# Kernel tuning notes

Hardware: AMD Instinct MI355X
Metric: run time of the kernel (lower is better)

## Reference

```python
import jax, jax.numpy as jnp
import numpy as np

B, T, HU, C = 256, 128, 512, 64

def setup_inputs() -> dict:
    key = jax.random.key(0)
    k = jax.random.split(key, 8)
    H = jax.random.normal(k[0], (B, T, HU), dtype=jnp.float32)
    y = jax.random.randint(k[1], (B, T), 0, C)
    y_len = jax.random.randint(k[2], (B,), 1, T + 1).astype(jnp.int32)
    y_mask = (jnp.arange(T)[None, :] < y_len[:, None]).astype(jnp.float32)
    xav = float(np.sqrt(6.0 / (3 * HU + C)))
    W = jax.random.uniform(k[3], (C, 3 * HU), minval=-xav, maxval=xav, dtype=jnp.float32)
    b = jnp.zeros((C,), dtype=jnp.float32)
    start_transitions = jax.random.uniform(k[4], (C,), minval=-1.0, maxval=1.0, dtype=jnp.float32)
    end_transitions = jax.random.uniform(k[5], (C,), minval=-1.0, maxval=1.0, dtype=jnp.float32)
    transitions = jax.random.uniform(k[6], (C, C), minval=-1.0, maxval=1.0, dtype=jnp.float32)
    return {"H": H, "W": W, "b": b, "start_transitions": start_transitions,
            "end_transitions": end_transitions, "transitions": transitions,
            "y": y, "y_mask": y_mask, "y_len": y_len}

def _crf_ll(H, W, b, start_transitions, end_transitions, transitions, y, y_mask, y_len):
    Bn, Tn, hu = H.shape
    zeros = jnp.zeros((Bn, 1, hu), H.dtype)
    prev = jnp.concatenate([zeros, H[:, :-1, :]], axis=1)
    nxt = jnp.concatenate([H[:, 1:, :], zeros], axis=1)
    context = jnp.concatenate([prev, H, nxt], axis=-1)            # [B,T,3h]
    scores = jnp.einsum('bth,ch->btc', context, W) + b            # [B,T,C]

    # numerator (gold path score)
    em_sel = jnp.take_along_axis(scores, y[..., None], axis=2)[..., 0]  # [B,T]
    num = start_transitions[y[:, 0]]
    num = num + jnp.sum(em_sel[:, :-1] * y_mask[:, :-1], axis=1)
    num = num + jnp.sum(transitions[y[:, :-1], y[:, 1:]] * y_mask[:, 1:], axis=1)
    last_tags = jnp.take_along_axis(y, (y_len - 1)[:, None].astype(y.dtype), axis=1)[:, 0]
    num = num + end_transitions[last_tags]
    num = num + jnp.take_along_axis(scores[:, -1, :], last_tags[:, None], axis=1)[:, 0] * y_mask[:, -1]

    # partition (log Z) via masked logsumexp scan
    em_t = jnp.transpose(scores, (1, 0, 2))   # [T,B,C]
    m_t = y_mask.T                            # [T,B]
    lp0 = start_transitions[None, :] + em_t[0]
    def step(lp, inp):
        em, m = inp
        new = jax.nn.logsumexp(lp[:, :, None] + transitions[None, :, :] + em[:, None, :], axis=1)
        lp = new * m[:, None] + lp * (1.0 - m[:, None])
        return lp, None
    lp, _ = jax.lax.scan(step, lp0, (em_t[1:], m_t[1:]))
    logZ = jax.nn.logsumexp(lp + end_transitions[None, :], axis=1)
    return num - logZ                          # [B]

def reference(H, W, b, start_transitions, end_transitions, transitions, y, y_mask, y_len):
    return _crf_ll(H, W, b, start_transitions, end_transitions, transitions, y, y_mask, y_len)
```

## Files before the change

kernel.cpp:

```cpp
#include <hip/hip_runtime.h>

typedef __attribute__((ext_vector_type(8))) short short8;
typedef __attribute__((ext_vector_type(4))) float f32x4;

__device__ __forceinline__ unsigned pk_rne(float a, float b) {
  unsigned short ha = __builtin_bit_cast(unsigned short, (_Float16)a);
  unsigned short hb = __builtin_bit_cast(unsigned short, (_Float16)b);
  return (unsigned)ha | ((unsigned)hb << 16);
}
__device__ __forceinline__ unsigned short f2bf(float x) {
  unsigned int u = __float_as_uint(x);
  u += 0x7FFFu + ((u >> 16) & 1u);
  return (unsigned short)(u >> 16);
}
__device__ __forceinline__ float bf2f(unsigned short h) {
  return __uint_as_float(((unsigned)h) << 16);
}
__device__ __forceinline__ unsigned pk_bf(float a, float b) {
  unsigned r;
  asm("v_cvt_pk_bf16_f32 %0, %1, %2" : "=v"(r) : "v"(a), "v"(b));
  return r;
}
__device__ __forceinline__ unsigned scale_bf_pair(unsigned w, float s) {
  float f0 = __uint_as_float(w << 16) * s;
  float f1 = __uint_as_float(w & 0xFFFF0000u) * s;
  return pk_bf(f0, f1);
}

__global__ __launch_bounds__(512) void crf_fused_kernel(
    const float* __restrict__ H, const float* __restrict__ W,
    const float* __restrict__ bias,
    const float* __restrict__ startT, const float* __restrict__ endT,
    const float* __restrict__ trans,
    const int* __restrict__ y, const int* __restrict__ y_len,
    float* __restrict__ out)
{
  __shared__ __align__(16) float smem[25088];
  __shared__ __align__(16) unsigned char EAbuf[8192];
  __shared__ __align__(16) float sc[128][68];
  __shared__ float scm[128];
  __shared__ float emy[128];
  __shared__ __align__(16) float ubuf[64];
  __shared__ float numsh;
  unsigned char* stg = (unsigned char*)smem;
  float* P = smem;
  unsigned char* Mbase = (unsigned char*)smem;

  const int b    = blockIdx.x;
  const int tid  = threadIdx.x;
  const int lane = tid & 63;
  const int wid  = tid >> 6;
  const int wm   = wid >> 2;
  const int wn   = wid & 3;

  f32x4 acc[4][3] = {};
  const float* Hb = H + (size_t)b * (128 * 512);
  const int len = y_len[b];
  const int* yb = y + b * 128;

  float4 areg[4], breg[6];
  int aRow[4], aK4[4], bN[6], bK4[6];
  #pragma unroll
  for (int it = 0; it < 4; ++it) { int i = it * 512 + tid; aRow[it] = i >> 4; aK4[it] = i & 15; }
  #pragma unroll
  for (int it = 0; it < 6; ++it) { int i = it * 512 + tid; bN[it] = i >> 4; bK4[it] = i & 15; }
  #pragma unroll
  for (int it = 0; it < 4; ++it)
    areg[it] = ((const float4*)(Hb + aRow[it] * 512))[aK4[it]];
  #pragma unroll
  for (int it = 0; it < 6; ++it)
    breg[it] = ((const float4*)(W + (bN[it] & 63) * 1536 + (bN[it] >> 6) * 512))[bK4[it]];

  #pragma unroll
  for (int it = 0; it < 2; ++it) {
    int idx = it * 512 + tid;
    int c = idx >> 4, c4 = idx & 15;
    float4 v = ((const float4*)trans)[idx];
    #pragma unroll
    for (int e = 0; e < 4; ++e) {
      int cp = c4 * 4 + e;
      float val = __expf(((const float*)&v)[e] - 1.0f);
      *(unsigned short*)(EAbuf + cp * 128 + ((2 * c) ^ ((cp & 7) << 4))) = f2bf(val);
    }
  }

  #pragma unroll
  for (int it = 0; it < 4; ++it) {
    float4 v = areg[it];
    uint2 o; o.x = pk_rne(v.x, v.y); o.y = pk_rne(v.z, v.w);
    *(uint2*)(stg + aRow[it] * 128 + ((aK4[it] * 8) ^ ((aRow[it] & 7) << 4))) = o;
  }
  #pragma unroll
  for (int it = 0; it < 6; ++it) {
    float4 v = breg[it];
    uint2 o; o.x = pk_rne(v.x, v.y); o.y = pk_rne(v.z, v.w);
    *(uint2*)(stg + 16384 + bN[it] * 128 + ((bK4[it] * 8) ^ ((bN[it] & 7) << 4))) = o;
  }
  __syncthreads();

  for (int kk = 0; kk < 8; ++kk) {
    unsigned char* aTc = stg + (kk & 1) * 40960;
    unsigned char* bTc = aTc + 16384;
    if (kk < 7) {
      #pragma unroll
      for (int it = 0; it < 4; ++it)
        areg[it] = ((const float4*)(Hb + aRow[it] * 512 + (kk + 1) * 64))[aK4[it]];
      #pragma unroll
      for (int it = 0; it < 6; ++it)
        breg[it] = ((const float4*)(W + (bN[it] & 63) * 1536 + (bN[it] >> 6) * 512 + (kk + 1) * 64))[bK4[it]];
    }
    #pragma unroll
    for (int ks = 0; ks < 2; ++ks) {
      const int kbyte = ks * 64 + ((lane >> 4) << 4);
      short8 ah[4], bh[3];
      #pragma unroll
      for (int m = 0; m < 4; ++m) {
        int row = wm * 64 + m * 16 + (lane & 15);
        ah[m] = *(const short8*)(aTc + row * 128 + (kbyte ^ ((row & 7) << 4)));
      }
      #pragma unroll
      for (int n = 0; n < 3; ++n) {
        int col = wn * 48 + n * 16 + (lane & 15);
        bh[n] = *(const short8*)(bTc + col * 128 + (kbyte ^ ((col & 7) << 4)));
      }
      #pragma unroll
      for (int m = 0; m < 4; ++m)
        #pragma unroll
        for (int n = 0; n < 3; ++n)
          asm("v_mfma_f32_16x16x32_f16 %0, %1, %2, %0"
              : "+v"(acc[m][n]) : "v"(ah[m]), "v"(bh[n]));
    }
    if (kk < 7) {
      unsigned char* aTn = stg + ((kk + 1) & 1) * 40960;
      unsigned char* bTn = aTn + 16384;
      #pragma unroll
      for (int it = 0; it < 4; ++it) {
        float4 v = areg[it];
        uint2 o; o.x = pk_rne(v.x, v.y); o.y = pk_rne(v.z, v.w);
        *(uint2*)(aTn + aRow[it] * 128 + ((aK4[it] * 8) ^ ((aRow[it] & 7) << 4))) = o;
      }
      #pragma unroll
      for (int it = 0; it < 6; ++it) {
        float4 v = breg[it];
        uint2 o; o.x = pk_rne(v.x, v.y); o.y = pk_rne(v.z, v.w);
        *(uint2*)(bTn + bN[it] * 128 + ((bK4[it] * 8) ^ ((bN[it] & 7) << 4))) = o;
      }
    }
    __syncthreads();
  }

  #pragma unroll
  for (int m = 0; m < 4; ++m)
    #pragma unroll
    for (int n = 0; n < 3; ++n) {
      int row0 = wm * 64 + m * 16 + ((lane >> 4) << 2);
      int col  = wn * 48 + n * 16 + (lane & 15);
      #pragma unroll
      for (int j = 0; j < 4; ++j)
        P[(row0 + j) * 196 + col] = acc[m][n][j];
    }
  __syncthreads();

  #pragma unroll
  for (int it = 0; it < 4; ++it) {
    int i4 = it * 512 + tid;
    int t = i4 >> 4, c4 = i4 & 15;
    float4 s = *(const float4*)(P + t * 196 + 64 + c4 * 4);
    float4 bb = ((const float4*)bias)[c4];
    s.x += bb.x; s.y += bb.y; s.z += bb.z; s.w += bb.w;
    if (t > 0) {
      float4 g = *(const float4*)(P + (t - 1) * 196 + c4 * 4);
      s.x += g.x; s.y += g.y; s.z += g.z; s.w += g.w;
    }
    if (t < 127) {
      float4 g = *(const float4*)(P + (t + 1) * 196 + 128 + c4 * 4);
      s.x += g.x; s.y += g.y; s.z += g.z; s.w += g.w;
    }
    float m4 = fmaxf(fmaxf(s.x, s.y), fmaxf(s.z, s.w));
    #pragma unroll
    for (int o = 1; o < 16; o <<= 1) m4 = fmaxf(m4, __shfl_xor(m4, o, 64));
    if ((lane & 15) == 0) scm[t] = m4;
    int yt = yb[t];
    if ((yt >> 2) == c4) {
      int r = yt & 3;
      emy[t] = (r == 0) ? s.x : (r == 1) ? s.y : (r == 2) ? s.z : s.w;
    }
    float4 e;
    e.x = __expf(s.x - m4); e.y = __expf(s.y - m4);
    e.z = __expf(s.z - m4); e.w = __expf(s.w - m4);
    *(float4*)(&sc[t][c4 * 4]) = e;
  }
  __syncthreads();

  if (wid == 7) {
    float p = 0.f;
    #pragma unroll
    for (int rep = 0; rep < 2; ++rep) {
      int t = lane + rep * 64;
      if (t < 127) {
        int yt = yb[t], yt1 = yb[t + 1];
        if (t < len)     p += emy[t];
        if (t + 1 < len) p += trans[yt * 64 + yt1];
      }
    }
    #pragma unroll
    for (int s = 32; s > 0; s >>= 1) p += __shfl_xor(p, s, 64);
    float nm = p + startT[yb[0]] + endT[yb[len - 1]];
    if (len == 128) nm += emy[127];
    if (lane == 0) numsh = nm;
  }

  {
    unsigned char* Mb = Mbase + wid * 8192;
    int t0 = (wid == 0) ? 1 : 16 * wid;
    int t1 = 16 * wid + 15; if (t1 > len - 1) t1 = len - 1;
    if (t0 <= t1) {
      const int sw = (lane & 7) << 4;
      float s0 = sc[t0][lane];
      #pragma unroll
      for (int j = 0; j < 8; ++j) {
        uint4 w = *(const uint4*)(EAbuf + lane * 128 + ((j * 16) ^ sw));
        uint4 o;
        o.x = scale_bf_pair(w.x, s0); o.y = scale_bf_pair(w.y, s0);
        o.z = scale_bf_pair(w.z, s0); o.w = scale_bf_pair(w.w, s0);
        *(uint4*)(Mb + lane * 128 + ((j * 16) ^ sw)) = o;
      }
      short8 ea[4][2];
      #pragma unroll
      for (int rt = 0; rt < 4; ++rt)
        #pragma unroll
        for (int kh = 0; kh < 2; ++kh) {
          int row = rt * 16 + (lane & 15);
          int kb = kh * 64 + ((lane >> 4) << 4);
          ea[rt][kh] = *(const short8*)(EAbuf + row * 128 + (kb ^ ((row & 7) << 4)));
        }
      f32x4 z4 = {0.f, 0.f, 0.f, 0.f};
      for (int t = t0 + 1; t <= t1; ++t) {
        short8 mf[4][2];
        #pragma unroll
        for (int ct = 0; ct < 4; ++ct)
          #pragma unroll
          for (int kh = 0; kh < 2; ++kh) {
            int row = ct * 16 + (lane & 15);
            int kb = kh * 64 + ((lane >> 4) << 4);
            mf[ct][kh] = *(const short8*)(Mb + row * 128 + (kb ^ ((row & 7) << 4)));
          }
        f32x4 sv[4];
        #pragma unroll
        for (int rt = 0; rt < 4; ++rt)
          sv[rt] = *(const f32x4*)(&sc[t][rt * 16 + ((lane >> 4) << 2)]);
        f32x4 c[4][4];
        #pragma unroll
        for (int rt = 0; rt < 4; ++rt)
          #pragma unroll
          for (int ct = 0; ct < 4; ++ct) {
            asm("v_mfma_f32_16x16x32_bf16 %0, %1, %2, %3"
                : "=&v"(c[rt][ct]) : "v"(ea[rt][0]), "v"(mf[ct][0]), "v"(z4));
            asm("v_mfma_f32_16x16x32_bf16 %0, %1, %2, %0"
                : "+v"(c[rt][ct]) : "v"(ea[rt][1]), "v"(mf[ct][1]));
          }
        #pragma unroll
        for (int rt = 0; rt < 4; ++rt)
          #pragma unroll
          for (int ct = 0; ct < 4; ++ct) {
            f32x4 cc = c[rt][ct] * sv[rt];
            uint2 w2; w2.x = pk_bf(cc[0], cc[1]); w2.y = pk_bf(cc[2], cc[3]);
            int row = ct * 16 + (lane & 15);
            int byt = 2 * (rt * 16 + ((lane >> 4) << 2));
            *(uint2*)(Mb + row * 128 + (byt ^ ((row & 7) << 4))) = w2;
          }
      }
    }
  }
  __syncthreads();
  if (wid != 0) return;

  float eE = __expf(endT[lane]);
  float ls;
  {
    int t1 = 1 + lane, t2 = 65 + lane;
    float a = (t1 <= len - 1) ? (scm[t1] + 1.0f) : 0.f;
    if (t2 <= len - 1) a += scm[t2] + 1.0f;
    #pragma unroll
    for (int s = 32; s > 0; s >>= 1) a += __shfl_xor(a, s, 64);
    ls = a + scm[0];
  }
  float u = __expf(startT[lane]) * sc[0][lane];

  for (int k = 0; k < 8; ++k) {
    if (k && 16 * k >= len) break;
    int lo = (k == 0) ? 1 : 16 * k;
    int hi = 16 * k + 15; if (hi > len - 1) hi = len - 1;
    if (lo > hi) continue;
    float r = u;
    #pragma unroll
    for (int s = 32; s > 0; s >>= 1) r = fmaxf(r, __shfl_xor(r, s, 64));
    unsigned br = __float_as_uint(r) & 0x7F800000u;
    u *= __uint_as_float(0x7F000000u - br);
    ls += (float)((int)(br >> 23) - 127) * 0.69314718055994531f;
    const unsigned char* Mb = Mbase + k * 8192;
    ubuf[lane] = u;
    float v0 = 0.f, v1 = 0.f, v2 = 0.f, v3 = 0.f;
    #pragma unroll 4
    for (int c = 0; c < 64; c += 4) {
      float4 uu = *(const float4*)&ubuf[c];
      float m0 = bf2f(*(const unsigned short*)(Mb + (c + 0) * 128 + ((2 * lane) ^ (((c + 0) & 7) << 4))));
      float m1 = bf2f(*(const unsigned short*)(Mb + (c + 1) * 128 + ((2 * lane) ^ (((c + 1) & 7) << 4))));
      float m2 = bf2f(*(const unsigned short*)(Mb + (c + 2) * 128 + ((2 * lane) ^ (((c + 2) & 7) << 4))));
      float m3 = bf2f(*(const unsigned short*)(Mb + (c + 3) * 128 + ((2 * lane) ^ (((c + 3) & 7) << 4))));
      v0 = fmaf(uu.x, m0, v0);
      v1 = fmaf(uu.y, m1, v1);
      v2 = fmaf(uu.z, m2, v2);
      v3 = fmaf(uu.w, m3, v3);
    }
    u = (v0 + v1) + (v2 + v3);
  }

  float x = u * eE;
  #pragma unroll
  for (int s = 32; s > 0; s >>= 1) x += __shfl_xor(x, s, 64);
  if (lane == 0) out[b] = numsh - (__logf(x) + ls);
}

extern "C" void kernel_launch(void* const* d_in, const int* in_sizes, int n_in,
                              void* d_out, int out_size, void* d_ws, size_t ws_size,
                              hipStream_t stream) {
  const float* H      = (const float*)d_in[0];
  const float* W      = (const float*)d_in[1];
  const float* bias   = (const float*)d_in[2];
  const float* startT = (const float*)d_in[3];
  const float* endT   = (const float*)d_in[4];
  const float* trans  = (const float*)d_in[5];
  const int*   y      = (const int*)d_in[6];
  const int*   y_len  = (const int*)d_in[8];
  float* out = (float*)d_out;

  crf_fused_kernel<<<dim3(256), dim3(512), 0, stream>>>(
      H, W, bias, startT, endT, trans, y, y_len, out);
}
```

Before: 43.86 us.

## Double block to 1024 threads, split GEMM rows and chunked scan columns across waves

```diff
diff --git a/kernel.cpp b/kernel.cpp
--- a/kernel.cpp
+++ b/kernel.cpp
@@ -27,7 +27,7 @@
   return pk_bf(f0, f1);
 }
 
-__global__ __launch_bounds__(512) void crf_fused_kernel(
+__global__ __launch_bounds__(1024) void crf_fused_kernel(
     const float* __restrict__ H, const float* __restrict__ W,
     const float* __restrict__ bias,
     const float* __restrict__ startT, const float* __restrict__ endT,
@@ -53,29 +53,27 @@
   const int wm   = wid >> 2;
   const int wn   = wid & 3;
 
-  f32x4 acc[4][3] = {};
+  f32x4 acc[2][3] = {};
   const float* Hb = H + (size_t)b * (128 * 512);
   const int len = y_len[b];
   const int* yb = y + b * 128;
 
-  float4 areg[4], breg[6];
-  int aRow[4], aK4[4], bN[6], bK4[6];
-  #pragma unroll
-  for (int it = 0; it < 4; ++it) { int i = it * 512 + tid; aRow[it] = i >> 4; aK4[it] = i & 15; }
-  #pragma unroll
-  for (int it = 0; it < 6; ++it) { int i = it * 512 + tid; bN[it] = i >> 4; bK4[it] = i & 15; }
-  #pragma unroll
-  for (int it = 0; it < 4; ++it)
+  float4 areg[2], breg[3];
+  int aRow[2], aK4[2], bN[3], bK4[3];
+  #pragma unroll
+  for (int it = 0; it < 2; ++it) { int i = it * 1024 + tid; aRow[it] = i >> 4; aK4[it] = i & 15; }
+  #pragma unroll
+  for (int it = 0; it < 3; ++it) { int i = it * 1024 + tid; bN[it] = i >> 4; bK4[it] = i & 15; }
+  #pragma unroll
+  for (int it = 0; it < 2; ++it)
     areg[it] = ((const float4*)(Hb + aRow[it] * 512))[aK4[it]];
   #pragma unroll
-  for (int it = 0; it < 6; ++it)
+  for (int it = 0; it < 3; ++it)
     breg[it] = ((const float4*)(W + (bN[it] & 63) * 1536 + (bN[it] >> 6) * 512))[bK4[it]];
 
-  #pragma unroll
-  for (int it = 0; it < 2; ++it) {
-    int idx = it * 512 + tid;
-    int c = idx >> 4, c4 = idx & 15;
-    float4 v = ((const float4*)trans)[idx];
+  {
+    int c = tid >> 4, c4 = tid & 15;
+    float4 v = ((const float4*)trans)[tid];
     #pragma unroll
     for (int e = 0; e < 4; ++e) {
       int cp = c4 * 4 + e;
@@ -85,13 +83,13 @@
   }
 
   #pragma unroll
-  for (int it = 0; it < 4; ++it) {
+  for (int it = 0; it < 2; ++it) {
     float4 v = areg[it];
     uint2 o; o.x = pk_rne(v.x, v.y); o.y = pk_rne(v.z, v.w);
     *(uint2*)(stg + aRow[it] * 128 + ((aK4[it] * 8) ^ ((aRow[it] & 7) << 4))) = o;
   }
   #pragma unroll
-  for (int it = 0; it < 6; ++it) {
+  for (int it = 0; it < 3; ++it) {
     float4 v = breg[it];
     uint2 o; o.x = pk_rne(v.x, v.y); o.y = pk_rne(v.z, v.w);
     *(uint2*)(stg + 16384 + bN[it] * 128 + ((bK4[it] * 8) ^ ((bN[it] & 7) << 4))) = o;
@@ -103,19 +101,19 @@
     unsigned char* bTc = aTc + 16384;
     if (kk < 7) {
       #pragma unroll
-      for (int it = 0; it < 4; ++it)
+      for (int it = 0; it < 2; ++it)
         areg[it] = ((const float4*)(Hb + aRow[it] * 512 + (kk + 1) * 64))[aK4[it]];
       #pragma unroll
-      for (int it = 0; it < 6; ++it)
+      for (int it = 0; it < 3; ++it)
         breg[it] = ((const float4*)(W + (bN[it] & 63) * 1536 + (bN[it] >> 6) * 512 + (kk + 1) * 64))[bK4[it]];
     }
     #pragma unroll
     for (int ks = 0; ks < 2; ++ks) {
       const int kbyte = ks * 64 + ((lane >> 4) << 4);
-      short8 ah[4], bh[3];
-      #pragma unroll
-      for (int m = 0; m < 4; ++m) {
-        int row = wm * 64 + m * 16 + (lane & 15);
+      short8 ah[2], bh[3];
+      #pragma unroll
+      for (int m = 0; m < 2; ++m) {
+        int row = wm * 32 + m * 16 + (lane & 15);
         ah[m] = *(const short8*)(aTc + row * 128 + (kbyte ^ ((row & 7) << 4)));
       }
       #pragma unroll
@@ -124,7 +122,7 @@
         bh[n] = *(const short8*)(bTc + col * 128 + (kbyte ^ ((col & 7) << 4)));
       }
       #pragma unroll
-      for (int m = 0; m < 4; ++m)
+      for (int m = 0; m < 2; ++m)
         #pragma unroll
         for (int n = 0; n < 3; ++n)
           asm("v_mfma_f32_16x16x32_f16 %0, %1, %2, %0"
@@ -134,13 +132,13 @@
       unsigned char* aTn = stg + ((kk + 1) & 1) * 40960;
       unsigned char* bTn = aTn + 16384;
       #pragma unroll
-      for (int it = 0; it < 4; ++it) {
+      for (int it = 0; it < 2; ++it) {
         float4 v = areg[it];
         uint2 o; o.x = pk_rne(v.x, v.y); o.y = pk_rne(v.z, v.w);
         *(uint2*)(aTn + aRow[it] * 128 + ((aK4[it] * 8) ^ ((aRow[it] & 7) << 4))) = o;
       }
       #pragma unroll
-      for (int it = 0; it < 6; ++it) {
+      for (int it = 0; it < 3; ++it) {
         float4 v = breg[it];
         uint2 o; o.x = pk_rne(v.x, v.y); o.y = pk_rne(v.z, v.w);
         *(uint2*)(bTn + bN[it] * 128 + ((bK4[it] * 8) ^ ((bN[it] & 7) << 4))) = o;
@@ -150,10 +148,10 @@
   }
 
   #pragma unroll
-  for (int m = 0; m < 4; ++m)
+  for (int m = 0; m < 2; ++m)
     #pragma unroll
     for (int n = 0; n < 3; ++n) {
-      int row0 = wm * 64 + m * 16 + ((lane >> 4) << 2);
+      int row0 = wm * 32 + m * 16 + ((lane >> 4) << 2);
       int col  = wn * 48 + n * 16 + (lane & 15);
       #pragma unroll
       for (int j = 0; j < 4; ++j)
@@ -162,8 +160,8 @@
   __syncthreads();
 
   #pragma unroll
-  for (int it = 0; it < 4; ++it) {
-    int i4 = it * 512 + tid;
+  for (int it = 0; it < 2; ++it) {
+    int i4 = it * 1024 + tid;
     int t = i4 >> 4, c4 = i4 & 15;
     float4 s = *(const float4*)(P + t * 196 + 64 + c4 * 4);
     float4 bb = ((const float4*)bias)[c4];
@@ -192,7 +190,7 @@
   }
   __syncthreads();
 
-  if (wid == 7) {
+  if (wid == 15) {
     float p = 0.f;
     #pragma unroll
     for (int rep = 0; rep < 2; ++rep) {
@@ -211,68 +209,81 @@
   }
 
   {
-    unsigned char* Mb = Mbase + wid * 8192;
-    int t0 = (wid == 0) ? 1 : 16 * wid;
-    int t1 = 16 * wid + 15; if (t1 > len - 1) t1 = len - 1;
+    const int cw = wid >> 1, side = wid & 1;
+    unsigned char* Mb = Mbase + cw * 8192;
+    int t0 = (cw == 0) ? 1 : 16 * cw;
+    int t1 = 16 * cw + 15; if (t1 > len - 1) t1 = len - 1;
+
     if (t0 <= t1) {
       const int sw = (lane & 7) << 4;
       float s0 = sc[t0][lane];
       #pragma unroll
-      for (int j = 0; j < 8; ++j) {
-        uint4 w = *(const uint4*)(EAbuf + lane * 128 + ((j * 16) ^ sw));
+      for (int j = 0; j < 4; ++j) {
+        int jj = side * 4 + j;
+        uint4 w = *(const uint4*)(EAbuf + lane * 128 + ((jj * 16) ^ sw));
         uint4 o;
         o.x = scale_bf_pair(w.x, s0); o.y = scale_bf_pair(w.y, s0);
         o.z = scale_bf_pair(w.z, s0); o.w = scale_bf_pair(w.w, s0);
-        *(uint4*)(Mb + lane * 128 + ((j * 16) ^ sw)) = o;
-      }
-      short8 ea[4][2];
+        *(uint4*)(Mb + lane * 128 + ((jj * 16) ^ sw)) = o;
+      }
+    }
+    short8 ea[4][2];
+    #pragma unroll
+    for (int rt = 0; rt < 4; ++rt)
+      #pragma unroll
+      for (int kh = 0; kh < 2; ++kh) {
+        int row = rt * 16 + (lane & 15);
+        int kb = kh * 64 + ((lane >> 4) << 4);
+        ea[rt][kh] = *(const short8*)(EAbuf + row * 128 + (kb ^ ((row & 7) << 4)));
+      }
+    f32x4 z4 = {0.f, 0.f, 0.f, 0.f};
+    __syncthreads();
+
+    #pragma unroll 1
+    for (int i = 1; i <= 15; ++i) {
+      int t = t0 + i;
+      bool active = (t <= t1);
+      short8 mf[2][2];
+      #pragma unroll
+      for (int cc = 0; cc < 2; ++cc) {
+        int ct = side * 2 + cc;
+        #pragma unroll
+        for (int kh = 0; kh < 2; ++kh) {
+          int row = ct * 16 + (lane & 15);
+          int kb = kh * 64 + ((lane >> 4) << 4);
+          mf[cc][kh] = *(const short8*)(Mb + row * 128 + (kb ^ ((row & 7) << 4)));
+        }
+      }
+      f32x4 sv[4];
+      #pragma unroll
+      for (int rt = 0; rt < 4; ++rt)
+        sv[rt] = *(const f32x4*)(&sc[t][rt * 16 + ((lane >> 4) << 2)]);
+      __syncthreads();
+      f32x4 c[4][2];
       #pragma unroll
       for (int rt = 0; rt < 4; ++rt)
         #pragma unroll
-        for (int kh = 0; kh < 2; ++kh) {
-          int row = rt * 16 + (lane & 15);
-          int kb = kh * 64 + ((lane >> 4) << 4);
-          ea[rt][kh] = *(const short8*)(EAbuf + row * 128 + (kb ^ ((row & 7) << 4)));
+        for (int cc = 0; cc < 2; ++cc) {
+          asm("v_mfma_f32_16x16x32_bf16 %0, %1, %2, %3"
+              : "=&v"(c[rt][cc]) : "v"(ea[rt][0]), "v"(mf[cc][0]), "v"(z4));
+          asm("v_mfma_f32_16x16x32_bf16 %0, %1, %2, %0"
+              : "+v"(c[rt][cc]) : "v"(ea[rt][1]), "v"(mf[cc][1]));
         }
-      f32x4 z4 = {0.f, 0.f, 0.f, 0.f};
-      for (int t = t0 + 1; t <= t1; ++t) {
-        short8 mf[4][2];
-        #pragma unroll
-        for (int ct = 0; ct < 4; ++ct)
-          #pragma unroll
-          for (int kh = 0; kh < 2; ++kh) {
-            int row = ct * 16 + (lane & 15);
-            int kb = kh * 64 + ((lane >> 4) << 4);
-            mf[ct][kh] = *(const short8*)(Mb + row * 128 + (kb ^ ((row & 7) << 4)));
-          }
-        f32x4 sv[4];
-        #pragma unroll
-        for (int rt = 0; rt < 4; ++rt)
-          sv[rt] = *(const f32x4*)(&sc[t][rt * 16 + ((lane >> 4) << 2)]);
-        f32x4 c[4][4];
+      if (active) {
         #pragma unroll
         for (int rt = 0; rt < 4; ++rt)
           #pragma unroll
-          for (int ct = 0; ct < 4; ++ct) {
-            asm("v_mfma_f32_16x16x32_bf16 %0, %1, %2, %3"
-                : "=&v"(c[rt][ct]) : "v"(ea[rt][0]), "v"(mf[ct][0]), "v"(z4));
-            asm("v_mfma_f32_16x16x32_bf16 %0, %1, %2, %0"
-                : "+v"(c[rt][ct]) : "v"(ea[rt][1]), "v"(mf[ct][1]));
-          }
-        #pragma unroll
-        for (int rt = 0; rt < 4; ++rt)
-          #pragma unroll
-          for (int ct = 0; ct < 4; ++ct) {
-            f32x4 cc = c[rt][ct] * sv[rt];
-            uint2 w2; w2.x = pk_bf(cc[0], cc[1]); w2.y = pk_bf(cc[2], cc[3]);
-            int row = ct * 16 + (lane & 15);
+          for (int cc = 0; cc < 2; ++cc) {
+            f32x4 v = c[rt][cc] * sv[rt];
+            uint2 w2; w2.x = pk_bf(v[0], v[1]); w2.y = pk_bf(v[2], v[3]);
+            int row = (side * 2 + cc) * 16 + (lane & 15);
             int byt = 2 * (rt * 16 + ((lane >> 4) << 2));
             *(uint2*)(Mb + row * 128 + (byt ^ ((row & 7) << 4))) = w2;
           }
       }
-    }
-  }
-  __syncthreads();
+      __syncthreads();
+    }
+  }
   if (wid != 0) return;
 
   float eE = __expf(endT[lane]);
@@ -335,6 +346,6 @@
   const int*   y_len  = (const int*)d_in[8];
   float* out = (float*)d_out;
 
-  crf_fused_kernel<<<dim3(256), dim3(512), 0, stream>>>(
+  crf_fused_kernel<<<dim3(256), dim3(1024), 0, stream>>>(
       H, W, bias, startT, endT, trans, y, y_len, out);
 }
```

After: 45.85 us. +4.5%, slower.
